# Optimization experiments

Measured on AMD Instinct MI355X. Metric: run time of the kernel, lower is better.

Reference implementation:

```python
import jax, jax.numpy as jnp
import numpy as np

D = 32  # embedding_dimension (TGN default memory_dimension == embedding_dimension)


def time_encode(t, w, b):
    # TGN TimeEncode: cos(t * w + b); t: [E] -> [E, D]
    return jnp.cos(t[:, None] * w[None, :] + b[None, :])


def setup_inputs() -> dict:
    key = jax.random.key(0)
    ks = jax.random.split(key, 24)
    N, B, E, F, NE = 1_000_000, 262_144, 1_048_576, 64, 500_000
    inp = {}
    # per-node-type memory tables (Mailbox memory)
    inp["mem_user"] = jax.random.normal(ks[0], (N, D), jnp.float32)
    inp["mem_item"] = jax.random.normal(ks[1], (N, D), jnp.float32)
    # active event node ids per type (memory lookup indices)
    inp["node_ids_user"] = jax.random.randint(ks[2], (B,), 0, N, jnp.int32)
    inp["node_ids_item"] = jax.random.randint(ks[3], (B,), 0, N, jnp.int32)
    # heterogeneous edge lists: user->item and item->user (indices into the B active nodes)
    inp["edge_src_ui"] = jax.random.randint(ks[4], (E,), 0, B, jnp.int32)
    inp["edge_dst_ui"] = jax.random.randint(ks[5], (E,), 0, B, jnp.int32)
    inp["edge_src_iu"] = jax.random.randint(ks[6], (E,), 0, B, jnp.int32)
    inp["edge_dst_iu"] = jax.random.randint(ks[7], (E,), 0, B, jnp.int32)
    inp["edge_idx_ui"] = jax.random.randint(ks[8], (E,), 0, NE, jnp.int32)
    inp["edge_idx_iu"] = jax.random.randint(ks[9], (E,), 0, NE, jnp.int32)
    inp["edge_rel_times_ui"] = jax.random.uniform(ks[10], (E,), jnp.float32) * 1000.0
    inp["edge_rel_times_iu"] = jax.random.uniform(ks[11], (E,), jnp.float32) * 1000.0
    inp["edge_feature"] = jax.random.normal(ks[12], (NE, F), jnp.float32)
    # per-node-type Linear(D, D, bias=False) == self.lin[node_type]
    s = 1.0 / np.sqrt(D)
    inp["W_user"] = jax.random.normal(ks[13], (D, D), jnp.float32) * s
    inp["W_item"] = jax.random.normal(ks[14], (D, D), jnp.float32) * s
    # per-edge-type Linear(F, D) == self.edge_feature_linear[edge_type]
    se = 1.0 / np.sqrt(F)
    inp["We_ui"] = jax.random.normal(ks[15], (F, D), jnp.float32) * se
    inp["be_ui"] = jnp.zeros((D,), jnp.float32)
    inp["We_iu"] = jax.random.normal(ks[16], (F, D), jnp.float32) * se
    inp["be_iu"] = jnp.zeros((D,), jnp.float32)
    # TimeEncode params (standard TGN init: 1/10^linspace)
    inp["time_w"] = jnp.asarray(1.0 / (10.0 ** np.linspace(0, 9, D)), jnp.float32)
    inp["time_b"] = jnp.zeros((D,), jnp.float32)
    # decoder(2*D -> 64 -> 16 -> 1), drop=0
    inp["dec_W1"] = jax.random.normal(ks[17], (2 * D, 64), jnp.float32) * (1.0 / np.sqrt(2 * D))
    inp["dec_b1"] = jnp.zeros((64,), jnp.float32)
    inp["dec_W2"] = jax.random.normal(ks[18], (64, 16), jnp.float32) * 0.125
    inp["dec_b2"] = jnp.zeros((16,), jnp.float32)
    inp["dec_W3"] = jax.random.normal(ks[19], (16, 1), jnp.float32) * 0.25
    inp["dec_b3"] = jnp.zeros((1,), jnp.float32)
    return inp


def reference(mem_user, mem_item, edge_feature, edge_rel_times_ui, edge_rel_times_iu,
              W_user, W_item, We_ui, be_ui, We_iu, be_iu, time_w, time_b,
              dec_W1, dec_b1, dec_W2, dec_b2, dec_W3, dec_b3,
              node_ids_user, node_ids_item, edge_src_ui, edge_dst_ui,
              edge_src_iu, edge_dst_iu, edge_idx_ui, edge_idx_iu):
    B = node_ids_user.shape[0]
    # memory lookup + per-node-type linear (self.lin[node_type], bias=False)
    h_user = mem_user[node_ids_user] @ W_user   # [B, D]
    h_item = mem_item[node_ids_item] @ W_item   # [B, D]
    # heterogeneous message passing: src memory + edge-feature linear + time encoding,
    # scattered (segment_sum) onto destination nodes per edge type
    msg_ui = (h_user[edge_src_ui]
              + edge_feature[edge_idx_ui] @ We_ui + be_ui
              + time_encode(edge_rel_times_ui, time_w, time_b))  # [E, D]
    agg_item = jax.ops.segment_sum(msg_ui, edge_dst_ui, num_segments=B)
    msg_iu = (h_item[edge_src_iu]
              + edge_feature[edge_idx_iu] @ We_iu + be_iu
              + time_encode(edge_rel_times_iu, time_w, time_b))  # [E, D]
    agg_user = jax.ops.segment_sum(msg_iu, edge_dst_iu, num_segments=B)
    hu = jax.nn.relu(h_user + agg_user)
    hi = jax.nn.relu(h_item + agg_item)
    # decoder `distance` on concatenated pair embeddings (2*D -> 64 -> 16 -> 1), drop=0
    z = jnp.concatenate([hu, hi], axis=-1)      # [B, 2D]
    x = jax.nn.relu(z @ dec_W1 + dec_b1)
    x = jax.nn.relu(x @ dec_W2 + dec_b2)
    return x @ dec_W3 + dec_b3                   # [B, 1]
```

## Files before the change

kernel.cpp:

```cpp
#include <hip/hip_runtime.h>

#define DEV __device__ __forceinline__

typedef __attribute__((ext_vector_type(8))) short short8;
typedef __attribute__((ext_vector_type(16))) float float16;

DEV unsigned short f2bf(float x) {
    unsigned u = __float_as_uint(x);
    unsigned r = (u + 0x7FFFu + ((u >> 16) & 1u)) >> 16;
    return (unsigned short)r;
}
DEV unsigned pack_bf2(float a, float b) {
    return (unsigned)f2bf(a) | ((unsigned)f2bf(b) << 16);
}
DEV float bf2f(unsigned short v) {
    return __uint_as_float(((unsigned)v) << 16);
}
DEV float fastcos(float x) {
    float r = x * 0.15915494309189535f;
    r = r - floorf(r);
    return __builtin_amdgcn_cosf(r);
}

__global__ void prep_kernel(const float* __restrict__ W_user, const float* __restrict__ W_item,
                            const float* __restrict__ We_ui, const float* __restrict__ be_ui,
                            const float* __restrict__ We_iu, const float* __restrict__ be_iu,
                            const float* __restrict__ dW1, const float* __restrict__ dW2,
                            float* __restrict__ Wt_user, float* __restrict__ Wt_item,
                            unsigned short* __restrict__ Wb, float* __restrict__ bc,
                            float* __restrict__ W1t, float* __restrict__ W2t) {
    int t = threadIdx.x;
    for (int i = t; i < 1024; i += 256) {
        int k = i / 32, d = i % 32;
        Wt_user[d * 32 + k] = W_user[i];
        Wt_item[d * 32 + k] = W_item[i];
    }
    for (int i = t; i < 4096; i += 256) {
        int kt   = i >> 10;
        int rem  = i & 1023;
        int n2   = rem >> 9;
        int rem2 = rem & 511;
        int l    = rem2 >> 3;
        int ii   = rem2 & 7;
        int k = kt * 16 + (l >> 5) * 8 + ii;
        int n = (l & 31);
        float v = n2 ? We_iu[k * 32 + n] : We_ui[k * 32 + n];
        Wb[i] = f2bf(v);
    }
    for (int i = t; i < 64; i += 256)
        bc[i] = (i < 32) ? be_ui[i] : be_iu[i - 32];
    for (int i = t; i < 4096; i += 256) {
        int j = i / 64, k = i % 64;
        W1t[i] = dW1[k * 64 + j];
    }
    for (int i = t; i < 1024; i += 256) {
        int c = i / 64, j = i % 64;
        W2t[i] = dW2[j * 16 + c];
    }
}

__global__ __launch_bounds__(256) void node_linear_kernel(
        const float* __restrict__ mem, const int* __restrict__ ids,
        const float* __restrict__ Wt, float* __restrict__ h, int B) {
    int r = blockIdx.x * 256 + threadIdx.x;
    if (r >= B) return;
    int id = ids[r];
    const float4* m4 = (const float4*)(mem + (size_t)id * 32);
    float m[32];
#pragma unroll
    for (int q = 0; q < 8; ++q) {
        float4 v = m4[q];
        m[4 * q + 0] = v.x; m[4 * q + 1] = v.y; m[4 * q + 2] = v.z; m[4 * q + 3] = v.w;
    }
    float* hr = h + (size_t)r * 32;
    for (int db = 0; db < 8; ++db) {
        float acc[4];
#pragma unroll
        for (int u = 0; u < 4; ++u) {
            const float* wr = Wt + (size_t)(db * 4 + u) * 32;
            float a = 0.f;
#pragma unroll
            for (int k = 0; k < 32; ++k) a = fmaf(m[k], wr[k], a);
            acc[u] = a;
        }
        float4 o; o.x = acc[0]; o.y = acc[1]; o.z = acc[2]; o.w = acc[3];
        *(float4*)(hr + db * 4) = o;
    }
}

__global__ __launch_bounds__(256) void proj_mfma_kernel(
        const float* __restrict__ feat, const unsigned short* __restrict__ Wb,
        const float* __restrict__ bc, unsigned short* __restrict__ proj, int NE) {
    __shared__ unsigned short lds[128 * 72];
    const int lane = threadIdx.x & 63;
    const int wave = threadIdx.x >> 6;
    const int col  = lane & 31;
    const int half = lane >> 5;

    short8 bfrag[8];
    const short8* wb8 = (const short8*)Wb;
#pragma unroll
    for (int f = 0; f < 8; ++f) bfrag[f] = wb8[f * 64 + lane];

    int r = blockIdx.x * 128 + wave * 32 + col;
    if (r >= NE) r = NE - 1;
    const float* fr = feat + (size_t)r * 64 + half * 8;
    short8 afrag[4];
#pragma unroll
    for (int t = 0; t < 4; ++t) {
        float4 a = *(const float4*)(fr + t * 16);
        float4 b = *(const float4*)(fr + t * 16 + 4);
        short8 s;
        s[0] = (short)f2bf(a.x); s[1] = (short)f2bf(a.y);
        s[2] = (short)f2bf(a.z); s[3] = (short)f2bf(a.w);
        s[4] = (short)f2bf(b.x); s[5] = (short)f2bf(b.y);
        s[6] = (short)f2bf(b.z); s[7] = (short)f2bf(b.w);
        afrag[t] = s;
    }

    float16 acc0, acc1;
    float b0 = bc[col], b1 = bc[32 + col];
#pragma unroll
    for (int i = 0; i < 16; ++i) { acc0[i] = b0; acc1[i] = b1; }
#pragma unroll
    for (int t = 0; t < 4; ++t) {
        acc0 = __builtin_amdgcn_mfma_f32_32x32x16_bf16(afrag[t], bfrag[t * 2 + 0], acc0, 0, 0, 0);
        acc1 = __builtin_amdgcn_mfma_f32_32x32x16_bf16(afrag[t], bfrag[t * 2 + 1], acc1, 0, 0, 0);
    }

#pragma unroll
    for (int reg = 0; reg < 16; ++reg) {
        int rl = wave * 32 + (reg & 3) + 8 * (reg >> 2) + 4 * half;
        lds[rl * 72 + col]      = f2bf(acc0[reg]);
        lds[rl * 72 + 32 + col] = f2bf(acc1[reg]);
    }
    __syncthreads();

    int trow = threadIdx.x >> 1, thalf = threadIdx.x & 1;
    int grow = blockIdx.x * 128 + trow;
    if (grow < NE) {
        const uint4* lsrc = (const uint4*)(lds + trow * 72 + thalf * 32);
        uint4* gdst = (uint4*)(proj + (size_t)grow * 64 + thalf * 32);
#pragma unroll
        for (int s = 0; s < 4; ++s) gdst[s] = lsrc[s];
    }
}

__global__ __launch_bounds__(256) void edge_kernel(
        const int* __restrict__ src, const int* __restrict__ dst,
        const int* __restrict__ eidx, const float* __restrict__ rt,
        const float* __restrict__ h, const unsigned short* __restrict__ proj,
        float* __restrict__ agg,
        const float* __restrict__ tw, const float* __restrict__ tb, int E) {
    long long i = (long long)blockIdx.x * 256 + threadIdx.x;
    int e = (int)(i >> 5), d = (int)(i & 31);
    if (e >= E) return;
    int s = src[e], dd = dst[e], ix = eidx[e];
    float t = rt[e];
    float c = fastcos(fmaf(t, tw[d], tb[d]));
    float pv = bf2f(proj[(size_t)ix * 64 + d]);
    float m = h[(size_t)s * 32 + d] + pv + c;
    unsafeAtomicAdd(&agg[(size_t)dd * 32 + d], m);
}

__global__ __launch_bounds__(256) void decoder_kernel(
        const float* __restrict__ h_user, const float* __restrict__ h_item,
        const float* __restrict__ agg_user, const float* __restrict__ agg_item,
        const float* __restrict__ W1t, const float* __restrict__ b1,
        const float* __restrict__ W2t, const float* __restrict__ b2,
        const float* __restrict__ W3, const float* __restrict__ b3,
        float* __restrict__ out, int B) {
    int i = blockIdx.x * 256 + threadIdx.x;
    if (i >= B) return;
    float z[64];
    {
        const float4* a4 = (const float4*)(h_user + (size_t)i * 32);
        const float4* b4 = (const float4*)(agg_user + (size_t)i * 32);
#pragma unroll
        for (int q = 0; q < 8; ++q) {
            float4 a = a4[q], b = b4[q];
            z[4 * q + 0] = fmaxf(a.x + b.x, 0.f);
            z[4 * q + 1] = fmaxf(a.y + b.y, 0.f);
            z[4 * q + 2] = fmaxf(a.z + b.z, 0.f);
            z[4 * q + 3] = fmaxf(a.w + b.w, 0.f);
        }
    }
    {
        const float4* a4 = (const float4*)(h_item + (size_t)i * 32);
        const float4* b4 = (const float4*)(agg_item + (size_t)i * 32);
#pragma unroll
        for (int q = 0; q < 8; ++q) {
            float4 a = a4[q], b = b4[q];
            z[32 + 4 * q + 0] = fmaxf(a.x + b.x, 0.f);
            z[32 + 4 * q + 1] = fmaxf(a.y + b.y, 0.f);
            z[32 + 4 * q + 2] = fmaxf(a.z + b.z, 0.f);
            z[32 + 4 * q + 3] = fmaxf(a.w + b.w, 0.f);
        }
    }
    float x2[16];
#pragma unroll
    for (int c = 0; c < 16; ++c) x2[c] = b2[c];
    for (int jb = 0; jb < 8; ++jb) {
        float a[8];
#pragma unroll
        for (int u = 0; u < 8; ++u) {
            int j = jb * 8 + u;
            const float* wr = W1t + (size_t)j * 64;
            float acc = b1[j];
#pragma unroll
            for (int k = 0; k < 64; ++k) acc = fmaf(z[k], wr[k], acc);
            a[u] = fmaxf(acc, 0.f);
        }
#pragma unroll
        for (int c = 0; c < 16; ++c) {
            const float* w2r = W2t + (size_t)c * 64 + jb * 8;
            float acc = x2[c];
#pragma unroll
            for (int u = 0; u < 8; ++u) acc = fmaf(a[u], w2r[u], acc);
            x2[c] = acc;
        }
    }
    float o = b3[0];
#pragma unroll
    for (int c = 0; c < 16; ++c) o = fmaf(fmaxf(x2[c], 0.f), W3[c], o);
    out[i] = o;
}

extern "C" void kernel_launch(void* const* d_in, const int* in_sizes, int n_in,
                              void* d_out, int out_size, void* d_ws, size_t ws_size,
                              hipStream_t stream) {
    const float* mem_user = (const float*)d_in[0];
    const float* mem_item = (const float*)d_in[1];
    const int*   ids_user = (const int*)d_in[2];
    const int*   ids_item = (const int*)d_in[3];
    const int*   src_ui   = (const int*)d_in[4];
    const int*   dst_ui   = (const int*)d_in[5];
    const int*   src_iu   = (const int*)d_in[6];
    const int*   dst_iu   = (const int*)d_in[7];
    const int*   eidx_ui  = (const int*)d_in[8];
    const int*   eidx_iu  = (const int*)d_in[9];
    const float* rt_ui    = (const float*)d_in[10];
    const float* rt_iu    = (const float*)d_in[11];
    const float* feat     = (const float*)d_in[12];
    const float* W_user   = (const float*)d_in[13];
    const float* W_item   = (const float*)d_in[14];
    const float* We_ui    = (const float*)d_in[15];
    const float* be_ui    = (const float*)d_in[16];
    const float* We_iu    = (const float*)d_in[17];
    const float* be_iu    = (const float*)d_in[18];
    const float* tw       = (const float*)d_in[19];
    const float* tb       = (const float*)d_in[20];
    const float* dW1      = (const float*)d_in[21];
    const float* db1      = (const float*)d_in[22];
    const float* dW2      = (const float*)d_in[23];
    const float* db2      = (const float*)d_in[24];
    const float* dW3      = (const float*)d_in[25];
    const float* db3      = (const float*)d_in[26];

    const int B  = in_sizes[2];
    const int E  = in_sizes[4];
    const int NE = in_sizes[12] / 64;

    float* w = (float*)d_ws;
    const size_t hsz = (size_t)B * 32;
    float* h_user   = w;
    float* h_item   = h_user + hsz;
    float* agg_user = h_item + hsz;
    float* agg_item = agg_user + hsz;
    float* Wt_user  = agg_item + hsz;
    float* Wt_item  = Wt_user + 1024;
    unsigned short* Wb = (unsigned short*)(Wt_item + 1024);
    float* bc       = (float*)(Wb + 4096);
    float* W1t      = bc + 64;
    float* W2t      = W1t + 4096;
    unsigned short* proj = (unsigned short*)(W2t + 1024);

    prep_kernel<<<1, 256, 0, stream>>>(W_user, W_item, We_ui, be_ui, We_iu, be_iu, dW1, dW2,
                                       Wt_user, Wt_item, Wb, bc, W1t, W2t);
    node_linear_kernel<<<(B + 255) / 256, 256, 0, stream>>>(mem_user, ids_user, Wt_user, h_user, B);
    node_linear_kernel<<<(B + 255) / 256, 256, 0, stream>>>(mem_item, ids_item, Wt_item, h_item, B);
    hipMemsetAsync(agg_user, 0, 2 * hsz * sizeof(float), stream);
    proj_mfma_kernel<<<(NE + 127) / 128, 256, 0, stream>>>(feat, Wb, bc, proj, NE);

    long long tot = (long long)E * 32;
    int eblocks = (int)((tot + 255) / 256);
    edge_kernel<<<eblocks, 256, 0, stream>>>(src_ui, dst_ui, eidx_ui, rt_ui,
                                             h_user, proj + 0, agg_item, tw, tb, E);
    edge_kernel<<<eblocks, 256, 0, stream>>>(src_iu, dst_iu, eidx_iu, rt_iu,
                                             h_item, proj + 32, agg_user, tw, tb, E);
    decoder_kernel<<<(B + 255) / 256, 256, 0, stream>>>(h_user, h_item, agg_user, agg_item,
                                                        W1t, db1, W2t, db2, dW3, db3,
                                                        (float*)d_out, B);
}
```

Before: 801.0 us.

## Replace atomic scatter with CSR counting-sort and per-destination gather aggregation

Edges are bucketed by destination node with a histogram, a three-stage prefix scan and a permute, so that a gather kernel can sum each node's messages in registers, add its own h, apply ReLU and write the result with no float atomics. Node hidden states are now stored as bf16 to halve gather traffic, and the decoder reads the precomputed ReLU outputs directly. The aim is to remove 64M scattered float atomics on the aggregation buffer and the memset. In exchange it adds several kernels, atomic counters in the histogram and permute, scattered writes during the permute, extra workspace, and bf16 rounding of h. The grid sizes (B/256, 2E/256) assume exact divisibility.

```diff
diff --git a/kernel.cpp b/kernel.cpp
--- a/kernel.cpp
+++ b/kernel.cpp
@@ -61,7 +61,7 @@
 
 __global__ __launch_bounds__(256) void node_linear_kernel(
         const float* __restrict__ mem, const int* __restrict__ ids,
-        const float* __restrict__ Wt, float* __restrict__ h, int B) {
+        const float* __restrict__ Wt, unsigned short* __restrict__ h, int B) {
     int r = blockIdx.x * 256 + threadIdx.x;
     if (r >= B) return;
     int id = ids[r];
@@ -72,19 +72,26 @@
         float4 v = m4[q];
         m[4 * q + 0] = v.x; m[4 * q + 1] = v.y; m[4 * q + 2] = v.z; m[4 * q + 3] = v.w;
     }
-    float* hr = h + (size_t)r * 32;
+    float o32[32];
     for (int db = 0; db < 8; ++db) {
-        float acc[4];
 #pragma unroll
         for (int u = 0; u < 4; ++u) {
             const float* wr = Wt + (size_t)(db * 4 + u) * 32;
             float a = 0.f;
 #pragma unroll
             for (int k = 0; k < 32; ++k) a = fmaf(m[k], wr[k], a);
-            acc[u] = a;
-        }
-        float4 o; o.x = acc[0]; o.y = acc[1]; o.z = acc[2]; o.w = acc[3];
-        *(float4*)(hr + db * 4) = o;
+            o32[db * 4 + u] = a;
+        }
+    }
+    uint4* hr = (uint4*)(h + (size_t)r * 32);
+#pragma unroll
+    for (int q = 0; q < 4; ++q) {
+        uint4 p;
+        p.x = pack_bf2(o32[8 * q + 0], o32[8 * q + 1]);
+        p.y = pack_bf2(o32[8 * q + 2], o32[8 * q + 3]);
+        p.z = pack_bf2(o32[8 * q + 4], o32[8 * q + 5]);
+        p.w = pack_bf2(o32[8 * q + 6], o32[8 * q + 7]);
+        hr[q] = p;
     }
 }
 
@@ -146,26 +153,121 @@
     }
 }
 
-__global__ __launch_bounds__(256) void edge_kernel(
-        const int* __restrict__ src, const int* __restrict__ dst,
-        const int* __restrict__ eidx, const float* __restrict__ rt,
-        const float* __restrict__ h, const unsigned short* __restrict__ proj,
-        float* __restrict__ agg,
-        const float* __restrict__ tw, const float* __restrict__ tb, int E) {
-    long long i = (long long)blockIdx.x * 256 + threadIdx.x;
-    int e = (int)(i >> 5), d = (int)(i & 31);
-    if (e >= E) return;
-    int s = src[e], dd = dst[e], ix = eidx[e];
-    float t = rt[e];
-    float c = fastcos(fmaf(t, tw[d], tb[d]));
-    float pv = bf2f(proj[(size_t)ix * 64 + d]);
-    float m = h[(size_t)s * 32 + d] + pv + c;
-    unsafeAtomicAdd(&agg[(size_t)dd * 32 + d], m);
+__global__ __launch_bounds__(256) void hist_kernel(
+        const int* __restrict__ dst_ui, const int* __restrict__ dst_iu,
+        int* __restrict__ cnt, int E, int B) {
+    int i = blockIdx.x * 256 + threadIdx.x;
+    if (i < E) atomicAdd(&cnt[dst_ui[i]], 1);
+    else       atomicAdd(&cnt[B + dst_iu[i - E]], 1);
+}
+
+__global__ __launch_bounds__(256) void scanA_kernel(
+        const int* __restrict__ cnt, int* __restrict__ off, int* __restrict__ bsum) {
+    __shared__ int s[256];
+    int t = threadIdx.x;
+    int i = blockIdx.x * 256 + t;
+    int v = cnt[i];
+    s[t] = v; __syncthreads();
+#pragma unroll
+    for (int o = 1; o < 256; o <<= 1) {
+        int x = (t >= o) ? s[t - o] : 0;
+        __syncthreads();
+        s[t] += x;
+        __syncthreads();
+    }
+    off[i] = s[t] - v;
+    if (t == 255) bsum[blockIdx.x] = s[255];
+}
+
+__global__ __launch_bounds__(256) void scanB_kernel(
+        const int* __restrict__ bsum, int* __restrict__ bscan) {
+    __shared__ int s[256];
+    int t = threadIdx.x;
+    for (int seg = 0; seg < 2; ++seg) {
+        int base = seg * 1024;
+        int v[4]; int tot = 0;
+#pragma unroll
+        for (int k = 0; k < 4; ++k) { v[k] = bsum[base + t * 4 + k]; tot += v[k]; }
+        s[t] = tot; __syncthreads();
+#pragma unroll
+        for (int o = 1; o < 256; o <<= 1) {
+            int x = (t >= o) ? s[t - o] : 0;
+            __syncthreads();
+            s[t] += x;
+            __syncthreads();
+        }
+        int run = s[t] - tot;
+#pragma unroll
+        for (int k = 0; k < 4; ++k) { bscan[base + t * 4 + k] = run; run += v[k]; }
+        __syncthreads();
+    }
+}
+
+__global__ __launch_bounds__(256) void scanC_kernel(
+        int* __restrict__ off, const int* __restrict__ bscan, int* __restrict__ cur) {
+    int i = blockIdx.x * 256 + threadIdx.x;
+    int o = off[i] + bscan[blockIdx.x];
+    off[i] = o;
+    cur[i] = o;
+}
+
+__global__ __launch_bounds__(256) void permute_kernel(
+        const int* __restrict__ src_ui, const int* __restrict__ dst_ui,
+        const int* __restrict__ eidx_ui, const float* __restrict__ rt_ui,
+        const int* __restrict__ src_iu, const int* __restrict__ dst_iu,
+        const int* __restrict__ eidx_iu, const float* __restrict__ rt_iu,
+        int* __restrict__ cur,
+        int* __restrict__ ssrc_ui, int* __restrict__ seidx_ui, float* __restrict__ srt_ui,
+        int* __restrict__ ssrc_iu, int* __restrict__ seidx_iu, float* __restrict__ srt_iu,
+        int E, int B) {
+    int i = blockIdx.x * 256 + threadIdx.x;
+    if (i < E) {
+        int b = dst_ui[i];
+        int p = atomicAdd(&cur[b], 1);
+        ssrc_ui[p] = src_ui[i]; seidx_ui[p] = eidx_ui[i]; srt_ui[p] = rt_ui[i];
+    } else {
+        int k = i - E;
+        int b = dst_iu[k];
+        int p = atomicAdd(&cur[B + b], 1);
+        ssrc_iu[p] = src_iu[k]; seidx_iu[p] = eidx_iu[k]; srt_iu[p] = rt_iu[k];
+    }
+}
+
+__global__ __launch_bounds__(256) void gather_kernel(
+        const unsigned short* __restrict__ h_src, const unsigned short* __restrict__ h_self,
+        const unsigned short* __restrict__ proj,
+        const int* __restrict__ ssrc, const int* __restrict__ seidx, const float* __restrict__ srt,
+        const int* __restrict__ off, const int* __restrict__ cur,
+        const float* __restrict__ tw, const float* __restrict__ tb,
+        float* __restrict__ outz) {
+    int g = (blockIdx.x * 256 + threadIdx.x) >> 5;
+    int d = threadIdx.x & 31;
+    int start = off[g], end = cur[g];
+    float twd = tw[d], tbd = tb[d];
+    float acc = 0.f;
+    int j = start;
+    for (; j + 2 <= end; j += 2) {
+        int s0 = ssrc[j],  s1 = ssrc[j + 1];
+        int e0 = seidx[j], e1 = seidx[j + 1];
+        float t0 = srt[j], t1 = srt[j + 1];
+        float hv0 = bf2f(h_src[(size_t)s0 * 32 + d]);
+        float hv1 = bf2f(h_src[(size_t)s1 * 32 + d]);
+        float p0 = bf2f(proj[(size_t)e0 * 64 + d]);
+        float p1 = bf2f(proj[(size_t)e1 * 64 + d]);
+        acc += hv0 + p0 + fastcos(fmaf(t0, twd, tbd));
+        acc += hv1 + p1 + fastcos(fmaf(t1, twd, tbd));
+    }
+    if (j < end) {
+        int s0 = ssrc[j]; int e0 = seidx[j]; float t0 = srt[j];
+        acc += bf2f(h_src[(size_t)s0 * 32 + d]) + bf2f(proj[(size_t)e0 * 64 + d])
+             + fastcos(fmaf(t0, twd, tbd));
+    }
+    float hs = bf2f(h_self[(size_t)g * 32 + d]);
+    outz[(size_t)g * 32 + d] = fmaxf(hs + acc, 0.f);
 }
 
 __global__ __launch_bounds__(256) void decoder_kernel(
-        const float* __restrict__ h_user, const float* __restrict__ h_item,
-        const float* __restrict__ agg_user, const float* __restrict__ agg_item,
+        const float* __restrict__ hu, const float* __restrict__ hi,
         const float* __restrict__ W1t, const float* __restrict__ b1,
         const float* __restrict__ W2t, const float* __restrict__ b2,
         const float* __restrict__ W3, const float* __restrict__ b3,
@@ -174,27 +276,20 @@
     if (i >= B) return;
     float z[64];
     {
-        const float4* a4 = (const float4*)(h_user + (size_t)i * 32);
-        const float4* b4 = (const float4*)(agg_user + (size_t)i * 32);
+        const float4* a4 = (const float4*)(hu + (size_t)i * 32);
 #pragma unroll
         for (int q = 0; q < 8; ++q) {
-            float4 a = a4[q], b = b4[q];
-            z[4 * q + 0] = fmaxf(a.x + b.x, 0.f);
-            z[4 * q + 1] = fmaxf(a.y + b.y, 0.f);
-            z[4 * q + 2] = fmaxf(a.z + b.z, 0.f);
-            z[4 * q + 3] = fmaxf(a.w + b.w, 0.f);
+            float4 a = a4[q];
+            z[4 * q + 0] = a.x; z[4 * q + 1] = a.y; z[4 * q + 2] = a.z; z[4 * q + 3] = a.w;
         }
     }
     {
-        const float4* a4 = (const float4*)(h_item + (size_t)i * 32);
-        const float4* b4 = (const float4*)(agg_item + (size_t)i * 32);
+        const float4* a4 = (const float4*)(hi + (size_t)i * 32);
 #pragma unroll
         for (int q = 0; q < 8; ++q) {
-            float4 a = a4[q], b = b4[q];
-            z[32 + 4 * q + 0] = fmaxf(a.x + b.x, 0.f);
-            z[32 + 4 * q + 1] = fmaxf(a.y + b.y, 0.f);
-            z[32 + 4 * q + 2] = fmaxf(a.z + b.z, 0.f);
-            z[32 + 4 * q + 3] = fmaxf(a.w + b.w, 0.f);
+            float4 a = a4[q];
+            z[32 + 4 * q + 0] = a.x; z[32 + 4 * q + 1] = a.y;
+            z[32 + 4 * q + 2] = a.z; z[32 + 4 * q + 3] = a.w;
         }
     }
     float x2[16];
@@ -261,34 +356,55 @@
     const int E  = in_sizes[4];
     const int NE = in_sizes[12] / 64;
 
-    float* w = (float*)d_ws;
+    char* w = (char*)d_ws;
     const size_t hsz = (size_t)B * 32;
-    float* h_user   = w;
-    float* h_item   = h_user + hsz;
-    float* agg_user = h_item + hsz;
-    float* agg_item = agg_user + hsz;
-    float* Wt_user  = agg_item + hsz;
-    float* Wt_item  = Wt_user + 1024;
-    unsigned short* Wb = (unsigned short*)(Wt_item + 1024);
-    float* bc       = (float*)(Wb + 4096);
-    float* W1t      = bc + 64;
-    float* W2t      = W1t + 4096;
-    unsigned short* proj = (unsigned short*)(W2t + 1024);
+    float* hu = (float*)w;                        w += hsz * 4;
+    float* hi = (float*)w;                        w += hsz * 4;
+    unsigned short* h_user_bf = (unsigned short*)w; w += hsz * 2;
+    unsigned short* h_item_bf = (unsigned short*)w; w += hsz * 2;
+    unsigned short* proj = (unsigned short*)w;    w += (size_t)NE * 64 * 2;
+    int*   ssrc_ui  = (int*)w;   w += (size_t)E * 4;
+    int*   seidx_ui = (int*)w;   w += (size_t)E * 4;
+    float* srt_ui   = (float*)w; w += (size_t)E * 4;
+    int*   ssrc_iu  = (int*)w;   w += (size_t)E * 4;
+    int*   seidx_iu = (int*)w;   w += (size_t)E * 4;
+    float* srt_iu   = (float*)w; w += (size_t)E * 4;
+    int*   cnt = (int*)w;  w += (size_t)2 * B * 4;
+    int*   cur = (int*)w;  w += (size_t)2 * B * 4;
+    int*   off = (int*)w;  w += (size_t)2 * B * 4;
+    int*   bsum  = (int*)w; w += 2048 * 4;
+    int*   bscan = (int*)w; w += 2048 * 4;
+    float* Wt_user = (float*)w; w += 1024 * 4;
+    float* Wt_item = (float*)w; w += 1024 * 4;
+    unsigned short* Wb = (unsigned short*)w; w += 4096 * 2;
+    float* bc  = (float*)w; w += 64 * 4;
+    float* W1t = (float*)w; w += 4096 * 4;
+    float* W2t = (float*)w; w += 1024 * 4;
 
     prep_kernel<<<1, 256, 0, stream>>>(W_user, W_item, We_ui, be_ui, We_iu, be_iu, dW1, dW2,
                                        Wt_user, Wt_item, Wb, bc, W1t, W2t);
-    node_linear_kernel<<<(B + 255) / 256, 256, 0, stream>>>(mem_user, ids_user, Wt_user, h_user, B);
-    node_linear_kernel<<<(B + 255) / 256, 256, 0, stream>>>(mem_item, ids_item, Wt_item, h_item, B);
-    hipMemsetAsync(agg_user, 0, 2 * hsz * sizeof(float), stream);
+    node_linear_kernel<<<B / 256, 256, 0, stream>>>(mem_user, ids_user, Wt_user, h_user_bf, B);
+    node_linear_kernel<<<B / 256, 256, 0, stream>>>(mem_item, ids_item, Wt_item, h_item_bf, B);
     proj_mfma_kernel<<<(NE + 127) / 128, 256, 0, stream>>>(feat, Wb, bc, proj, NE);
 
-    long long tot = (long long)E * 32;
-    int eblocks = (int)((tot + 255) / 256);
-    edge_kernel<<<eblocks, 256, 0, stream>>>(src_ui, dst_ui, eidx_ui, rt_ui,
-                                             h_user, proj + 0, agg_item, tw, tb, E);
-    edge_kernel<<<eblocks, 256, 0, stream>>>(src_iu, dst_iu, eidx_iu, rt_iu,
-                                             h_item, proj + 32, agg_user, tw, tb, E);
-    decoder_kernel<<<(B + 255) / 256, 256, 0, stream>>>(h_user, h_item, agg_user, agg_item,
-                                                        W1t, db1, W2t, db2, dW3, db3,
-                                                        (float*)d_out, B);
-}
+    hipMemsetAsync(cnt, 0, (size_t)2 * B * 4, stream);
+    hist_kernel<<<2 * E / 256, 256, 0, stream>>>(dst_ui, dst_iu, cnt, E, B);
+    scanA_kernel<<<2 * B / 256, 256, 0, stream>>>(cnt, off, bsum);
+    scanB_kernel<<<1, 256, 0, stream>>>(bsum, bscan);
+    scanC_kernel<<<2 * B / 256, 256, 0, stream>>>(off, bscan, cur);
+    permute_kernel<<<2 * E / 256, 256, 0, stream>>>(src_ui, dst_ui, eidx_ui, rt_ui,
+                                                    src_iu, dst_iu, eidx_iu, rt_iu,
+                                                    cur,
+                                                    ssrc_ui, seidx_ui, srt_ui,
+                                                    ssrc_iu, seidx_iu, srt_iu, E, B);
+
+    gather_kernel<<<B * 32 / 256, 256, 0, stream>>>(h_user_bf, h_item_bf, proj + 0,
+                                                    ssrc_ui, seidx_ui, srt_ui,
+                                                    off, cur, tw, tb, hi);
+    gather_kernel<<<B * 32 / 256, 256, 0, stream>>>(h_item_bf, h_user_bf, proj + 32,
+                                                    ssrc_iu, seidx_iu, srt_iu,
+                                                    off + B, cur + B, tw, tb, hu);
+
+    decoder_kernel<<<B / 256, 256, 0, stream>>>(hu, hi, W1t, db1, W2t, db2, dW3, db3,
+                                                (float*)d_out, B);
+}
```

New measurement: 895.7 us. +11.8%, slower.

## Bucket edges by destination range and store node embeddings in bf16

Applied to the files above, without the earlier changes.

Adds a histogram, scan and append pass that sorts edges into 32 destination buckets, packed as int4 records, per edge type. Bucket processing is mapped to XCDs via blockIdx so atomics to agg stay within a smaller, cache-resident range. Node embeddings h and the projected edge features are now stored as bf16 in separate per-type arrays, which halves gather traffic. The cost is extra passes over the edge arrays, more workspace, and lower precision in h. The grid sizes now assume B is divisible by 256.

```diff
diff --git a/kernel.cpp b/kernel.cpp
--- a/kernel.cpp
+++ b/kernel.cpp
@@ -61,7 +61,7 @@
 
 __global__ __launch_bounds__(256) void node_linear_kernel(
         const float* __restrict__ mem, const int* __restrict__ ids,
-        const float* __restrict__ Wt, float* __restrict__ h, int B) {
+        const float* __restrict__ Wt, unsigned short* __restrict__ h, int B) {
     int r = blockIdx.x * 256 + threadIdx.x;
     if (r >= B) return;
     int id = ids[r];
@@ -72,25 +72,33 @@
         float4 v = m4[q];
         m[4 * q + 0] = v.x; m[4 * q + 1] = v.y; m[4 * q + 2] = v.z; m[4 * q + 3] = v.w;
     }
-    float* hr = h + (size_t)r * 32;
+    float o32[32];
     for (int db = 0; db < 8; ++db) {
-        float acc[4];
 #pragma unroll
         for (int u = 0; u < 4; ++u) {
             const float* wr = Wt + (size_t)(db * 4 + u) * 32;
             float a = 0.f;
 #pragma unroll
             for (int k = 0; k < 32; ++k) a = fmaf(m[k], wr[k], a);
-            acc[u] = a;
-        }
-        float4 o; o.x = acc[0]; o.y = acc[1]; o.z = acc[2]; o.w = acc[3];
-        *(float4*)(hr + db * 4) = o;
+            o32[db * 4 + u] = a;
+        }
+    }
+    uint4* hr = (uint4*)(h + (size_t)r * 32);
+#pragma unroll
+    for (int q = 0; q < 4; ++q) {
+        uint4 p;
+        p.x = pack_bf2(o32[8 * q + 0], o32[8 * q + 1]);
+        p.y = pack_bf2(o32[8 * q + 2], o32[8 * q + 3]);
+        p.z = pack_bf2(o32[8 * q + 4], o32[8 * q + 5]);
+        p.w = pack_bf2(o32[8 * q + 6], o32[8 * q + 7]);
+        hr[q] = p;
     }
 }
 
 __global__ __launch_bounds__(256) void proj_mfma_kernel(
         const float* __restrict__ feat, const unsigned short* __restrict__ Wb,
-        const float* __restrict__ bc, unsigned short* __restrict__ proj, int NE) {
+        const float* __restrict__ bc,
+        unsigned short* __restrict__ proj_ui, unsigned short* __restrict__ proj_iu, int NE) {
     __shared__ unsigned short lds[128 * 72];
     const int lane = threadIdx.x & 63;
     const int wave = threadIdx.x >> 6;
@@ -136,35 +144,116 @@
     }
     __syncthreads();
 
-    int trow = threadIdx.x >> 1, thalf = threadIdx.x & 1;
+    int trow = threadIdx.x >> 1, tpl = threadIdx.x & 1;
     int grow = blockIdx.x * 128 + trow;
     if (grow < NE) {
-        const uint4* lsrc = (const uint4*)(lds + trow * 72 + thalf * 32);
-        uint4* gdst = (uint4*)(proj + (size_t)grow * 64 + thalf * 32);
+        const uint4* lsrc = (const uint4*)(lds + trow * 72 + tpl * 32);
+        unsigned short* gp = (tpl ? proj_iu : proj_ui) + (size_t)grow * 32;
+        uint4* gdst = (uint4*)gp;
 #pragma unroll
         for (int s = 0; s < 4; ++s) gdst[s] = lsrc[s];
     }
 }
 
-__global__ __launch_bounds__(256) void edge_kernel(
-        const int* __restrict__ src, const int* __restrict__ dst,
-        const int* __restrict__ eidx, const float* __restrict__ rt,
-        const float* __restrict__ h, const unsigned short* __restrict__ proj,
-        float* __restrict__ agg,
-        const float* __restrict__ tw, const float* __restrict__ tb, int E) {
-    long long i = (long long)blockIdx.x * 256 + threadIdx.x;
-    int e = (int)(i >> 5), d = (int)(i & 31);
-    if (e >= E) return;
-    int s = src[e], dd = dst[e], ix = eidx[e];
-    float t = rt[e];
-    float c = fastcos(fmaf(t, tw[d], tb[d]));
-    float pv = bf2f(proj[(size_t)ix * 64 + d]);
-    float m = h[(size_t)s * 32 + d] + pv + c;
-    unsafeAtomicAdd(&agg[(size_t)dd * 32 + d], m);
+__global__ __launch_bounds__(256) void hist_kernel(
+        const int* __restrict__ dst_ui, const int* __restrict__ dst_iu,
+        int* __restrict__ gcnt, int E) {
+    __shared__ int cnt[64];
+    int t = threadIdx.x;
+    if (t < 64) cnt[t] = 0;
+    __syncthreads();
+    long long chunk = (long long)blockIdx.x * 2048;
+#pragma unroll
+    for (int k = 0; k < 8; ++k) {
+        long long i = chunk + t + k * 256;
+        int b;
+        if (i < E) b = dst_ui[i] >> 13;
+        else       b = 32 + (dst_iu[i - E] >> 13);
+        atomicAdd(&cnt[b], 1);
+    }
+    __syncthreads();
+    if (t < 64) atomicAdd(&gcnt[t], cnt[t]);
+}
+
+__global__ void scan_kernel(const int* __restrict__ gcnt,
+                            int* __restrict__ gcur, int* __restrict__ bstart) {
+    if (threadIdx.x == 0) {
+        int acc = 0;
+        for (int b = 0; b < 32; ++b) { bstart[b] = acc; gcur[b] = acc; acc += gcnt[b]; }
+        acc = 0;
+        for (int b = 32; b < 64; ++b) { bstart[b] = acc; gcur[b] = acc; acc += gcnt[b]; }
+    }
+}
+
+__global__ __launch_bounds__(256) void append_kernel(
+        const int* __restrict__ dst_ui, const int* __restrict__ src_ui,
+        const int* __restrict__ eidx_ui, const float* __restrict__ rt_ui,
+        const int* __restrict__ dst_iu, const int* __restrict__ src_iu,
+        const int* __restrict__ eidx_iu, const float* __restrict__ rt_iu,
+        int* __restrict__ gcur, int4* __restrict__ recs_ui, int4* __restrict__ recs_iu, int E) {
+    __shared__ int cnt[64], gbase[64], lcur[64];
+    int t = threadIdx.x;
+    if (t < 64) { cnt[t] = 0; lcur[t] = 0; }
+    __syncthreads();
+    long long chunk = (long long)blockIdx.x * 2048;
+    int4 r[8]; int bb[8];
+#pragma unroll
+    for (int k = 0; k < 8; ++k) {
+        long long i = chunk + t + k * 256;
+        int4 v; int b;
+        if (i < E) {
+            v.x = dst_ui[i]; v.y = src_ui[i]; v.z = eidx_ui[i];
+            v.w = __float_as_int(rt_ui[i]);
+            b = v.x >> 13;
+        } else {
+            long long q = i - E;
+            v.x = dst_iu[q]; v.y = src_iu[q]; v.z = eidx_iu[q];
+            v.w = __float_as_int(rt_iu[q]);
+            b = 32 + (v.x >> 13);
+        }
+        r[k] = v; bb[k] = b;
+        atomicAdd(&cnt[b], 1);
+    }
+    __syncthreads();
+    if (t < 64) gbase[t] = atomicAdd(&gcur[t], cnt[t]);
+    __syncthreads();
+#pragma unroll
+    for (int k = 0; k < 8; ++k) {
+        int b = bb[k];
+        int p = gbase[b] + atomicAdd(&lcur[b], 1);
+        if (b < 32) recs_ui[p] = r[k];
+        else        recs_iu[p] = r[k];
+    }
+}
+
+__global__ __launch_bounds__(256) void edge_bucket_kernel(
+        const int4* __restrict__ recs, const unsigned short* __restrict__ h_src,
+        const unsigned short* __restrict__ projT, float* __restrict__ agg,
+        const float* __restrict__ tw, const float* __restrict__ tb,
+        const int* __restrict__ bstart, const int* __restrict__ gcur, int bkoff) {
+    const int d = threadIdx.x & 31;
+    const int group = threadIdx.x >> 5;
+    const int xcd = blockIdx.x & 7, bslot = blockIdx.x >> 3;
+    const float twd = tw[d], tbd = tb[d];
+    const int RUN = 64;
+    for (int bk = xcd; bk < 32; bk += 8) {
+        const int s = bstart[bkoff + bk], e = gcur[bkoff + bk];
+        for (int j0 = s + (bslot * 8 + group) * RUN; j0 < e; j0 += 256 * 8 * RUN) {
+            int je = min(e, j0 + RUN);
+#pragma unroll 2
+            for (int j = j0; j < je; ++j) {
+                int4 r = recs[j];
+                float hv = bf2f(h_src[(size_t)r.y * 32 + d]);
+                float pv = bf2f(projT[(size_t)r.z * 32 + d]);
+                float c = fastcos(fmaf(__int_as_float(r.w), twd, tbd));
+                unsafeAtomicAdd(&agg[(size_t)r.x * 32 + d], hv + pv + c);
+            }
+        }
+    }
 }
 
 __global__ __launch_bounds__(256) void decoder_kernel(
-        const float* __restrict__ h_user, const float* __restrict__ h_item,
+        const unsigned short* __restrict__ h_user, const unsigned short* __restrict__ h_item,
         const float* __restrict__ agg_user, const float* __restrict__ agg_item,
         const float* __restrict__ W1t, const float* __restrict__ b1,
         const float* __restrict__ W2t, const float* __restrict__ b2,
@@ -174,27 +263,39 @@
     if (i >= B) return;
     float z[64];
     {
-        const float4* a4 = (const float4*)(h_user + (size_t)i * 32);
-        const float4* b4 = (const float4*)(agg_user + (size_t)i * 32);
-#pragma unroll
-        for (int q = 0; q < 8; ++q) {
-            float4 a = a4[q], b = b4[q];
-            z[4 * q + 0] = fmaxf(a.x + b.x, 0.f);
-            z[4 * q + 1] = fmaxf(a.y + b.y, 0.f);
-            z[4 * q + 2] = fmaxf(a.z + b.z, 0.f);
-            z[4 * q + 3] = fmaxf(a.w + b.w, 0.f);
+        const uint4* h4 = (const uint4*)(h_user + (size_t)i * 32);
+        const float4* a4 = (const float4*)(agg_user + (size_t)i * 32);
+#pragma unroll
+        for (int q = 0; q < 4; ++q) {
+            uint4 hp = h4[q];
+            float4 a0 = a4[2 * q], a1 = a4[2 * q + 1];
+            unsigned hw[4] = {hp.x, hp.y, hp.z, hp.w};
+            float av[8] = {a0.x, a0.y, a0.z, a0.w, a1.x, a1.y, a1.z, a1.w};
+#pragma unroll
+            for (int u = 0; u < 4; ++u) {
+                float lo = __uint_as_float(hw[u] << 16);
+                float hi2 = __uint_as_float(hw[u] & 0xFFFF0000u);
+                z[8 * q + 2 * u]     = fmaxf(lo + av[2 * u], 0.f);
+                z[8 * q + 2 * u + 1] = fmaxf(hi2 + av[2 * u + 1], 0.f);
+            }
         }
     }
     {
-        const float4* a4 = (const float4*)(h_item + (size_t)i * 32);
-        const float4* b4 = (const float4*)(agg_item + (size_t)i * 32);
-#pragma unroll
-        for (int q = 0; q < 8; ++q) {
-            float4 a = a4[q], b = b4[q];
-            z[32 + 4 * q + 0] = fmaxf(a.x + b.x, 0.f);
-            z[32 + 4 * q + 1] = fmaxf(a.y + b.y, 0.f);
-            z[32 + 4 * q + 2] = fmaxf(a.z + b.z, 0.f);
-            z[32 + 4 * q + 3] = fmaxf(a.w + b.w, 0.f);
+        const uint4* h4 = (const uint4*)(h_item + (size_t)i * 32);
+        const float4* a4 = (const float4*)(agg_item + (size_t)i * 32);
+#pragma unroll
+        for (int q = 0; q < 4; ++q) {
+            uint4 hp = h4[q];
+            float4 a0 = a4[2 * q], a1 = a4[2 * q + 1];
+            unsigned hw[4] = {hp.x, hp.y, hp.z, hp.w};
+            float av[8] = {a0.x, a0.y, a0.z, a0.w, a1.x, a1.y, a1.z, a1.w};
+#pragma unroll
+            for (int u = 0; u < 4; ++u) {
+                float lo = __uint_as_float(hw[u] << 16);
+                float hi2 = __uint_as_float(hw[u] & 0xFFFF0000u);
+                z[32 + 8 * q + 2 * u]     = fmaxf(lo + av[2 * u], 0.f);
+                z[32 + 8 * q + 2 * u + 1] = fmaxf(hi2 + av[2 * u + 1], 0.f);
+            }
         }
     }
     float x2[16];
@@ -261,34 +362,47 @@
     const int E  = in_sizes[4];
     const int NE = in_sizes[12] / 64;
 
-    float* w = (float*)d_ws;
+    char* w = (char*)d_ws;
     const size_t hsz = (size_t)B * 32;
-    float* h_user   = w;
-    float* h_item   = h_user + hsz;
-    float* agg_user = h_item + hsz;
-    float* agg_item = agg_user + hsz;
-    float* Wt_user  = agg_item + hsz;
-    float* Wt_item  = Wt_user + 1024;
-    unsigned short* Wb = (unsigned short*)(Wt_item + 1024);
-    float* bc       = (float*)(Wb + 4096);
-    float* W1t      = bc + 64;
-    float* W2t      = W1t + 4096;
-    unsigned short* proj = (unsigned short*)(W2t + 1024);
+    unsigned short* h_user_bf = (unsigned short*)w; w += hsz * 2;
+    unsigned short* h_item_bf = (unsigned short*)w; w += hsz * 2;
+    unsigned short* proj_ui = (unsigned short*)w;   w += (size_t)NE * 32 * 2;
+    unsigned short* proj_iu = (unsigned short*)w;   w += (size_t)NE * 32 * 2;
+    int4* recs_ui = (int4*)w;  w += (size_t)E * 16;
+    int4* recs_iu = (int4*)w;  w += (size_t)E * 16;
+    float* agg_user = (float*)w; w += hsz * 4;
+    float* agg_item = (float*)w; w += hsz * 4;
+    int* gcnt   = (int*)w; w += 64 * 4;
+    int* gcur   = (int*)w; w += 64 * 4;
+    int* bstart = (int*)w; w += 64 * 4;
+    float* Wt_user = (float*)w; w += 1024 * 4;
+    float* Wt_item = (float*)w; w += 1024 * 4;
+    unsigned short* Wb = (unsigned short*)w; w += 4096 * 2;
+    float* bc  = (float*)w; w += 64 * 4;
+    float* W1t = (float*)w; w += 4096 * 4;
+    float* W2t = (float*)w; w += 1024 * 4;
 
     prep_kernel<<<1, 256, 0, stream>>>(W_user, W_item, We_ui, be_ui, We_iu, be_iu, dW1, dW2,
                                        Wt_user, Wt_item, Wb, bc, W1t, W2t);
-    node_linear_kernel<<<(B + 255) / 256, 256, 0, stream>>>(mem_user, ids_user, Wt_user, h_user, B);
-    node_linear_kernel<<<(B + 255) / 256, 256, 0, stream>>>(mem_item, ids_item, Wt_item, h_item, B);
-    hipMemsetAsync(agg_user, 0, 2 * hsz * sizeof(float), stream);
-    proj_mfma_kernel<<<(NE + 127) / 128, 256, 0, stream>>>(feat, Wb, bc, proj, NE);
-
-    long long tot = (long long)E * 32;
-    int eblocks = (int)((tot + 255) / 256);
-    edge_kernel<<<eblocks, 256, 0, stream>>>(src_ui, dst_ui, eidx_ui, rt_ui,
-                                             h_user, proj + 0, agg_item, tw, tb, E);
-    edge_kernel<<<eblocks, 256, 0, stream>>>(src_iu, dst_iu, eidx_iu, rt_iu,
-                                             h_item, proj + 32, agg_user, tw, tb, E);
-    decoder_kernel<<<(B + 255) / 256, 256, 0, stream>>>(h_user, h_item, agg_user, agg_item,
-                                                        W1t, db1, W2t, db2, dW3, db3,
-                                                        (float*)d_out, B);
-}
+    node_linear_kernel<<<B / 256, 256, 0, stream>>>(mem_user, ids_user, Wt_user, h_user_bf, B);
+    node_linear_kernel<<<B / 256, 256, 0, stream>>>(mem_item, ids_item, Wt_item, h_item_bf, B);
+    proj_mfma_kernel<<<(NE + 127) / 128, 256, 0, stream>>>(feat, Wb, bc, proj_ui, proj_iu, NE);
+
+    hipMemsetAsync(gcnt, 0, 64 * 4, stream);
+    int nchunks = (2 * E + 2047) / 2048;
+    hist_kernel<<<nchunks, 256, 0, stream>>>(dst_ui, dst_iu, gcnt, E);
+    scan_kernel<<<1, 64, 0, stream>>>(gcnt, gcur, bstart);
+    append_kernel<<<nchunks, 256, 0, stream>>>(dst_ui, src_ui, eidx_ui, rt_ui,
+                                               dst_iu, src_iu, eidx_iu, rt_iu,
+                                               gcur, recs_ui, recs_iu, E);
+
+    hipMemsetAsync(agg_user, 0, 2 * hsz * 4, stream);
+    edge_bucket_kernel<<<2048, 256, 0, stream>>>(recs_ui, h_user_bf, proj_ui, agg_item,
+                                                 tw, tb, bstart, gcur, 0);
+    edge_bucket_kernel<<<2048, 256, 0, stream>>>(recs_iu, h_item_bf, proj_iu, agg_user,
+                                                 tw, tb, bstart, gcur, 32);
+
+    decoder_kernel<<<B / 256, 256, 0, stream>>>(h_user_bf, h_item_bf, agg_user, agg_item,
+                                                W1t, db1, W2t, db2, dW3, db3,
+                                                (float*)d_out, B);
+}
```

New measurement: 865.0 us. +8.0%, slower.
